# Kernel tuning notes

Measured on AMD Instinct MI355X. Metric: run time of the kernel, lower is better.

Reference implementation:

```python
import jax, jax.numpy as jnp
import numpy as np

ANGLE_DEG = 15.0  # matches init_kwargs angle; cv2 convention: positive = counter-clockwise


def setup_inputs() -> dict:
    key = jax.random.key(0)
    encode_image = jax.random.normal(key, (32, 3, 512, 512), dtype=jnp.float32)
    return {"encode_image": encode_image}


def _rotate(img, angle_deg):
    """Faithful jax version of cv2.getRotationMatrix2D + cv2.warpAffine
    (INTER_LINEAR, BORDER_CONSTANT=0, scale=1), batched over B,C.
    cv2.warpAffine inverts M, so dst(x,y) = src(R(-angle) @ (x-c, y-c) + c).
    """
    B, C, H, W = img.shape
    theta = jnp.float32(angle_deg * np.pi / 180.0)
    a, b = jnp.cos(theta), jnp.sin(theta)
    # original code uses center (H//2, W//2) with dsize (H, W); square images assumed
    cx = jnp.float32(H // 2)
    cy = jnp.float32(W // 2)
    X, Y = jnp.meshgrid(jnp.arange(W, dtype=jnp.float32),
                        jnp.arange(H, dtype=jnp.float32))  # [H, W] dst pixel coords
    # inverse rotation (R(angle)^-1 = R(-angle)) about center
    xs = a * (X - cx) - b * (Y - cy) + cx  # src column coord
    ys = b * (X - cx) + a * (Y - cy) + cy  # src row coord
    x0 = jnp.floor(xs)
    y0 = jnp.floor(ys)
    wx = xs - x0
    wy = ys - y0
    x0i = x0.astype(jnp.int32)
    y0i = y0.astype(jnp.int32)

    def tap(yi, xi, w):
        # per-tap border-constant-0 handling, as cv2 BORDER_CONSTANT does
        valid = (xi >= 0) & (xi <= W - 1) & (yi >= 0) & (yi <= H - 1)
        xc = jnp.clip(xi, 0, W - 1)
        yc = jnp.clip(yi, 0, H - 1)
        vals = img[:, :, yc, xc]  # gather -> [B, C, H, W]
        return vals * (w * valid)[None, None]

    out = (tap(y0i,     x0i,     (1 - wy) * (1 - wx))
         + tap(y0i,     x0i + 1, (1 - wy) * wx)
         + tap(y0i + 1, x0i,     wy * (1 - wx))
         + tap(y0i + 1, x0i + 1, wy * wx))
    return out


def reference(encode_image):
    return _rotate(encode_image, ANGLE_DEG)
```

## Files before the change

kernel.cpp:

```cpp
#include <hip/hip_runtime.h>


#define IMG_H 512
#define IMG_W 512
#define NPLANES 96
#define TS 64
#define LROWS 80
#define LCOLS 80
#define LSTRIDE 84

__global__ __launch_bounds__(256) void rot_kernel(const float* __restrict__ in,
                                                  float* __restrict__ out) {
    const float a = 0.96592582628906831f;
    const float b = 0.25881904510252074f;

    __shared__ float tile[LROWS * LSTRIDE];

    const int blk = blockIdx.x;
    const int tx = blk & 7;
    const int ty = (blk >> 3) & 7;
    const int bc = blk >> 6;
    const int X0 = tx * TS;
    const int Y0 = ty * TS;

    const float* __restrict__ src = in + (size_t)bc * (IMG_H * IMG_W);

    const float fx_lo = (float)X0 - 256.0f;
    const float fy_lo = (float)Y0 - 256.0f;
    const float fy_hi = (float)(Y0 + 63) - 256.0f;

    const float xs_min = a * fx_lo + (-b * fy_hi + 256.0f);
    const float ys_min = b * fx_lo + ( a * fy_lo + 256.0f);
    const int xs0 = (int)floorf(xs_min);
    const int ys0 = (int)floorf(ys_min);

    const int t = threadIdx.x;

#pragma unroll
    for (int it = 0; it < (LROWS * LCOLS) / 256; ++it) {
        const int idx = t + it * 256;
        const int r = idx / LCOLS;
        const int c = idx - r * LCOLS;
        const int gy = min(max(ys0 + r, 0), IMG_H - 1);
        const int gx = min(max(xs0 + c, 0), IMG_W - 1);
        tile[r * LSTRIDE + c] = src[gy * IMG_W + gx];
    }
    __syncthreads();

    const int col4 = (t & 15) << 2;
    const int row_base = t >> 4;
    float* __restrict__ dst = out + (size_t)bc * (IMG_H * IMG_W);

#pragma unroll
    for (int rr = 0; rr < 4; ++rr) {
        const int y = Y0 + row_base + (rr << 4);
        const float fy = (float)y - 256.0f;
        const float bxs = -b * fy + 256.0f;
        const float bys =  a * fy + 256.0f;

        float o[4];
#pragma unroll
        for (int k = 0; k < 4; ++k) {
            const int x = X0 + col4 + k;
            const float fx = (float)x - 256.0f;
            const float xs = a * fx + bxs;
            const float ys = b * fx + bys;

            const float x0f = floorf(xs);
            const float y0f = floorf(ys);
            const float wx = xs - x0f;
            const float wy = ys - y0f;
            const int x0 = (int)x0f;
            const int y0 = (int)y0f;

            const float vx0 = ((unsigned)x0       < IMG_W) ? 1.0f : 0.0f;
            const float vx1 = ((unsigned)(x0 + 1) < IMG_W) ? 1.0f : 0.0f;
            const float vy0 = ((unsigned)y0       < IMG_H) ? 1.0f : 0.0f;
            const float vy1 = ((unsigned)(y0 + 1) < IMG_H) ? 1.0f : 0.0f;

            const float w00 = (1.0f - wy) * (1.0f - wx) * vy0 * vx0;
            const float w01 = (1.0f - wy) * wx          * vy0 * vx1;
            const float w10 = wy * (1.0f - wx)          * vy1 * vx0;
            const float w11 = wy * wx                   * vy1 * vx1;

            const int lr = y0 - ys0;
            const int lc = x0 - xs0;
            const float* __restrict__ p = &tile[lr * LSTRIDE + lc];
            const float v00 = p[0];
            const float v01 = p[1];
            const float v10 = p[LSTRIDE];
            const float v11 = p[LSTRIDE + 1];

            o[k] = v00 * w00 + v01 * w01 + v10 * w10 + v11 * w11;
        }
        *reinterpret_cast<float4*>(&dst[y * IMG_W + X0 + col4]) =
            make_float4(o[0], o[1], o[2], o[3]);
    }
}

extern "C" void kernel_launch(void* const* d_in, const int* in_sizes, int n_in,
                              void* d_out, int out_size, void* d_ws, size_t ws_size,
                              hipStream_t stream) {
    const float* in = (const float*)d_in[0];
    float* out = (float*)d_out;

    const int grid = NPLANES * (IMG_H / TS) * (IMG_W / TS);
    rot_kernel<<<grid, 256, 0, stream>>>(in, out);
}
```

Before: 216.1 us.

## Load source tile via direct global-to-LDS 16-byte loads and specialize interior tiles

```diff
diff --git a/kernel.cpp b/kernel.cpp
--- a/kernel.cpp
+++ b/kernel.cpp
@@ -6,51 +6,20 @@
 #define NPLANES 96
 #define TS 64
 #define LROWS 80
-#define LCOLS 80
-#define LSTRIDE 84
+#define LCOLS 84
+#define NGROUPS 1792
+#define LDS_FLOATS (NGROUPS * 4)
 
-__global__ __launch_bounds__(256) void rot_kernel(const float* __restrict__ in,
-                                                  float* __restrict__ out) {
-    const float a = 0.96592582628906831f;
-    const float b = 0.25881904510252074f;
+typedef __attribute__((address_space(1))) const float gfloat;
+typedef __attribute__((address_space(3))) float sfloat;
 
-    __shared__ float tile[LROWS * LSTRIDE];
-
-    const int blk = blockIdx.x;
-    const int tx = blk & 7;
-    const int ty = (blk >> 3) & 7;
-    const int bc = blk >> 6;
-    const int X0 = tx * TS;
-    const int Y0 = ty * TS;
-
-    const float* __restrict__ src = in + (size_t)bc * (IMG_H * IMG_W);
-
-    const float fx_lo = (float)X0 - 256.0f;
-    const float fy_lo = (float)Y0 - 256.0f;
-    const float fy_hi = (float)(Y0 + 63) - 256.0f;
-
-    const float xs_min = a * fx_lo + (-b * fy_hi + 256.0f);
-    const float ys_min = b * fx_lo + ( a * fy_lo + 256.0f);
-    const int xs0 = (int)floorf(xs_min);
-    const int ys0 = (int)floorf(ys_min);
-
-    const int t = threadIdx.x;
-
-#pragma unroll
-    for (int it = 0; it < (LROWS * LCOLS) / 256; ++it) {
-        const int idx = t + it * 256;
-        const int r = idx / LCOLS;
-        const int c = idx - r * LCOLS;
-        const int gy = min(max(ys0 + r, 0), IMG_H - 1);
-        const int gx = min(max(xs0 + c, 0), IMG_W - 1);
-        tile[r * LSTRIDE + c] = src[gy * IMG_W + gx];
-    }
-    __syncthreads();
-
+template <bool MASKED>
+__device__ __forceinline__ void compute_tile(const float* __restrict__ tile,
+                                             float* __restrict__ dst,
+                                             int X0, int Y0, int xs0a, int ys0,
+                                             int t, float a, float b) {
     const int col4 = (t & 15) << 2;
     const int row_base = t >> 4;
-    float* __restrict__ dst = out + (size_t)bc * (IMG_H * IMG_W);
-
 #pragma unroll
     for (int rr = 0; rr < 4; ++rr) {
         const int y = Y0 + row_base + (rr << 4);
@@ -73,28 +42,87 @@
             const int x0 = (int)x0f;
             const int y0 = (int)y0f;
 
-            const float vx0 = ((unsigned)x0       < IMG_W) ? 1.0f : 0.0f;
-            const float vx1 = ((unsigned)(x0 + 1) < IMG_W) ? 1.0f : 0.0f;
-            const float vy0 = ((unsigned)y0       < IMG_H) ? 1.0f : 0.0f;
-            const float vy1 = ((unsigned)(y0 + 1) < IMG_H) ? 1.0f : 0.0f;
+            float w00 = (1.0f - wy) * (1.0f - wx);
+            float w01 = (1.0f - wy) * wx;
+            float w10 = wy * (1.0f - wx);
+            float w11 = wy * wx;
 
-            const float w00 = (1.0f - wy) * (1.0f - wx) * vy0 * vx0;
-            const float w01 = (1.0f - wy) * wx          * vy0 * vx1;
-            const float w10 = wy * (1.0f - wx)          * vy1 * vx0;
-            const float w11 = wy * wx                   * vy1 * vx1;
+            if (MASKED) {
+                const float vx0 = ((unsigned)x0       < IMG_W) ? 1.0f : 0.0f;
+                const float vx1 = ((unsigned)(x0 + 1) < IMG_W) ? 1.0f : 0.0f;
+                const float vy0 = ((unsigned)y0       < IMG_H) ? 1.0f : 0.0f;
+                const float vy1 = ((unsigned)(y0 + 1) < IMG_H) ? 1.0f : 0.0f;
+                w00 *= vy0 * vx0;
+                w01 *= vy0 * vx1;
+                w10 *= vy1 * vx0;
+                w11 *= vy1 * vx1;
+            }
 
             const int lr = y0 - ys0;
-            const int lc = x0 - xs0;
-            const float* __restrict__ p = &tile[lr * LSTRIDE + lc];
+            const int lc = x0 - xs0a;
+            const float* __restrict__ p = &tile[lr * LCOLS + lc];
             const float v00 = p[0];
             const float v01 = p[1];
-            const float v10 = p[LSTRIDE];
-            const float v11 = p[LSTRIDE + 1];
+            const float v10 = p[LCOLS];
+            const float v11 = p[LCOLS + 1];
 
             o[k] = v00 * w00 + v01 * w01 + v10 * w10 + v11 * w11;
         }
         *reinterpret_cast<float4*>(&dst[y * IMG_W + X0 + col4]) =
             make_float4(o[0], o[1], o[2], o[3]);
+    }
+}
+
+__global__ __launch_bounds__(256) void rot_kernel(const float* __restrict__ in,
+                                                  float* __restrict__ out) {
+    const float a = 0.96592582628906831f;
+    const float b = 0.25881904510252074f;
+
+    __shared__ float tile[LDS_FLOATS];
+
+    const int blk = blockIdx.x;
+    const int tx = blk & 7;
+    const int ty = (blk >> 3) & 7;
+    const int bc = blk >> 6;
+    const int X0 = tx * TS;
+    const int Y0 = ty * TS;
+
+    const float fx_lo = (float)X0 - 256.0f;
+    const float fy_lo = (float)Y0 - 256.0f;
+    const float fy_hi = (float)(Y0 + 63) - 256.0f;
+    const float xs_min = a * fx_lo + (-b * fy_hi + 256.0f);
+    const float ys_min = b * fx_lo + ( a * fy_lo + 256.0f);
+    const int xs0  = (int)floorf(xs_min);
+    const int ys0  = (int)floorf(ys_min);
+    const int xs0a = xs0 & ~3;
+
+    const int t = threadIdx.x;
+    const int wave = t >> 6;
+    const int plane_base = bc * (IMG_H * IMG_W);
+    const int total = NPLANES * IMG_H * IMG_W;
+
+#pragma unroll
+    for (int it = 0; it < NGROUPS / 256; ++it) {
+        const int g = it * 256 + t;
+        const int r = g / 21;
+        const int c4 = (g - r * 21) << 2;
+        int gidx = plane_base + (ys0 + r) * IMG_W + xs0a + c4;
+        gidx = min(max(gidx, 0), total - 4);
+        __builtin_amdgcn_global_load_lds(
+            (gfloat*)(in + gidx),
+            (sfloat*)&tile[(it * 256 + (wave << 6)) * 4],
+            16, 0, 0);
+    }
+    __syncthreads();
+
+    float* __restrict__ dst = out + (size_t)bc * (IMG_H * IMG_W);
+
+    const bool interior = (xs0a >= 0) && (xs0a + LCOLS <= IMG_W) &&
+                          (ys0 >= 0) && (ys0 + LROWS <= IMG_H);
+    if (interior) {
+        compute_tile<false>(tile, dst, X0, Y0, xs0a, ys0, t, a, b);
+    } else {
+        compute_tile<true>(tile, dst, X0, Y0, xs0a, ys0, t, a, b);
     }
 }
 
```

Result: faster. 174.8 us (-19.1%).
